# Kernel optimization log

Hardware: AMD Instinct MI355X
Metric: run time of the kernel (lower is better)

The kernel has to match this reference:

```python
import jax, jax.numpy as jnp
import numpy as np

CHEB_K = 3  # from init_kwargs


def setup_inputs() -> dict:
    key = jax.random.key(0)
    k1, k2, k3, k4 = jax.random.split(key, 4)
    B, N, C_IN, C_OUT, D = 32, 4096, 32, 64, 16
    x = jax.random.normal(k1, (B, N, C_IN), dtype=jnp.float32)
    node_embeddings = jax.random.normal(k2, (N, D), dtype=jnp.float32)
    laplacian_mx = jnp.zeros((N, N), dtype=jnp.float32)  # unused by forward
    weights_pool = jax.random.normal(k3, (D, CHEB_K, C_IN, C_OUT), dtype=jnp.float32) * 0.1
    bias_pool = jax.random.normal(k4, (D, C_OUT), dtype=jnp.float32) * 0.1
    return {
        'x': x,
        'node_embeddings': node_embeddings,
        'laplacian_mx': laplacian_mx,
        'weights_pool': weights_pool,
        'bias_pool': bias_pool,
    }


def reference(x, node_embeddings, laplacian_mx, weights_pool, bias_pool):
    N = node_embeddings.shape[0]
    # adaptive adjacency: softmax(relu(E E^T)) over rows
    supports = jax.nn.softmax(jax.nn.relu(node_embeddings @ node_embeddings.T), axis=1)
    # Chebyshev recursion T_0=I, T_1=A, T_k = 2A T_{k-1} - T_{k-2}
    support_set = [jnp.eye(N, dtype=x.dtype), supports]
    for _ in range(2, CHEB_K):
        support_set.append(2.0 * supports @ support_set[-1] - support_set[-2])
    supports_k = jnp.stack(support_set, axis=0)  # [K, N, N]
    # per-node generated weights/bias
    weights = jnp.einsum('nd,dkio->nkio', node_embeddings, weights_pool)  # [N,K,I,O]
    bias = node_embeddings @ bias_pool  # [N, O]
    # graph propagation: [K,N,N] x [B,N,I] -> [B,K,N,I] -> [B,N,K,I]
    x_g = jnp.einsum('knm,bmc->bknc', supports_k, x).transpose(0, 2, 1, 3)
    # per-node grouped GEMM
    out = jnp.einsum('bnki,nkio->bno', x_g, weights) + bias
    return out
```

## Files before the change

kernel.cpp:

```cpp
#include <hip/hip_runtime.h>
#include <hip/hip_bf16.h>

#define N_NODES 4096
#define BATCH   32
#define CIN     32
#define COUT    64
#define DEMB    16
#define NCOL    (BATCH * CIN)
#define KIO     (3 * CIN * COUT)
#define SPLITK  3

typedef __bf16 bf16x8 __attribute__((ext_vector_type(8)));
typedef float  floatx4 __attribute__((ext_vector_type(4)));

__device__ inline void load_lds16(const void* g, void* l) {
    __builtin_amdgcn_global_load_lds(
        (const __attribute__((address_space(1))) void*)g,
        (__attribute__((address_space(3))) void*)l, 16, 0, 0);
}

__global__ __launch_bounds__(256) void compute_U_kernel(
        const float* __restrict__ E, __hip_bfloat16* __restrict__ U,
        float* __restrict__ invRow) {
    const int n0   = blockIdx.x * 8;
    const int t    = threadIdx.x;
    const int lane = t & 63, wave = t >> 6;
    __shared__ float red[4][8];

    float en[8][DEMB];
#pragma unroll
    for (int r = 0; r < 8; ++r) {
        const float4* er = (const float4*)&E[(size_t)(n0 + r) * DEMB];
        const float4 a0 = er[0], a1 = er[1], a2 = er[2], a3 = er[3];
        en[r][ 0]=a0.x; en[r][ 1]=a0.y; en[r][ 2]=a0.z; en[r][ 3]=a0.w;
        en[r][ 4]=a1.x; en[r][ 5]=a1.y; en[r][ 6]=a1.z; en[r][ 7]=a1.w;
        en[r][ 8]=a2.x; en[r][ 9]=a2.y; en[r][10]=a2.z; en[r][11]=a2.w;
        en[r][12]=a3.x; en[r][13]=a3.y; en[r][14]=a3.z; en[r][15]=a3.w;
    }

    float sum[8] = {0.f, 0.f, 0.f, 0.f, 0.f, 0.f, 0.f, 0.f};

    for (int tile = 0; tile < 16; ++tile) {
        const int c = tile * 256 + t;
        const float4* em4 = (const float4*)&E[(size_t)c * DEMB];
        const float4 b0 = em4[0], b1 = em4[1], b2 = em4[2], b3 = em4[3];
        float em[DEMB];
        em[ 0]=b0.x; em[ 1]=b0.y; em[ 2]=b0.z; em[ 3]=b0.w;
        em[ 4]=b1.x; em[ 5]=b1.y; em[ 6]=b1.z; em[ 7]=b1.w;
        em[ 8]=b2.x; em[ 9]=b2.y; em[10]=b2.z; em[11]=b2.w;
        em[12]=b3.x; em[13]=b3.y; em[14]=b3.z; em[15]=b3.w;
#pragma unroll
        for (int r = 0; r < 8; ++r) {
            float dt = 0.f;
#pragma unroll
            for (int d = 0; d < DEMB; ++d) dt += en[r][d] * em[d];
            const float ev = __expf(fmaxf(dt, 0.f));
            sum[r] += ev;
            U[(size_t)(n0 + r) * N_NODES + c] = __float2bfloat16(ev);
        }
    }
#pragma unroll
    for (int r = 0; r < 8; ++r)
#pragma unroll
        for (int off = 32; off > 0; off >>= 1) sum[r] += __shfl_xor(sum[r], off);
    if (lane == 0)
#pragma unroll
        for (int r = 0; r < 8; ++r) red[wave][r] = sum[r];
    __syncthreads();
    if (t < 8)
        invRow[n0 + t] = 1.0f / (red[0][t] + red[1][t] + red[2][t] + red[3][t]);
}

__global__ __launch_bounds__(256) void transpose_kernel(
        const float* __restrict__ x,
        __hip_bfloat16* __restrict__ Xt, __hip_bfloat16* __restrict__ Bt) {
    const int m0 = blockIdx.x * 64;
    const int b  = blockIdx.y;
    const int t  = threadIdx.x;
    __shared__ float tile[64][33];
    {
        const int ml = t >> 2, cg = (t & 3) * 8;
        const float* src = &x[((size_t)b * N_NODES + (m0 + ml)) * CIN + cg];
        const float4 r0 = *(const float4*)src;
        const float4 r1 = *(const float4*)(src + 4);
        tile[ml][cg+0] = r0.x; tile[ml][cg+1] = r0.y; tile[ml][cg+2] = r0.z; tile[ml][cg+3] = r0.w;
        tile[ml][cg+4] = r1.x; tile[ml][cg+5] = r1.y; tile[ml][cg+6] = r1.z; tile[ml][cg+7] = r1.w;
    }
    __syncthreads();
    {
        const int ml = t >> 2, cg = (t & 3) * 8;
        __hip_bfloat16* dst = &Xt[(size_t)(m0 + ml) * NCOL + b * CIN + cg];
#pragma unroll
        for (int j = 0; j < 8; ++j) dst[j] = __float2bfloat16(tile[ml][cg + j]);
    }
    {
        const int c = t >> 3, mg = (t & 7) * 8;
        __hip_bfloat16* dst = &Bt[(size_t)(b * CIN + c) * N_NODES + m0 + mg];
#pragma unroll
        for (int j = 0; j < 8; ++j) dst[j] = __float2bfloat16(tile[mg + j][c]);
    }
}

__global__ __launch_bounds__(256) void gen_w_kernel(
        const float* __restrict__ E, const float* __restrict__ Wp,
        __hip_bfloat16* __restrict__ Wn) {
    const int jc = blockIdx.x * 256;
    const int nc = blockIdx.y * 64;
    const int t  = threadIdx.x;
    __shared__ float wp[DEMB][256];
    __shared__ float et[64][DEMB];
#pragma unroll
    for (int d = 0; d < DEMB; ++d) wp[d][t] = Wp[(size_t)d * KIO + jc + t];
    ((float4*)et)[t] = ((const float4*)&E[(size_t)nc * DEMB])[t];
    __syncthreads();
    float w[DEMB];
#pragma unroll
    for (int d = 0; d < DEMB; ++d) w[d] = wp[d][t];
    for (int nl = 0; nl < 64; ++nl) {
        float acc = 0.0f;
#pragma unroll
        for (int d = 0; d < DEMB; ++d) acc += et[nl][d] * w[d];
        Wn[(size_t)(nc + nl) * KIO + jc + t] = __float2bfloat16(acc);
    }
}

__global__ __launch_bounds__(256) void gemm_splitk_kernel(
        const __hip_bfloat16* __restrict__ A,
        const __hip_bfloat16* __restrict__ Bt,
        __hip_bfloat16* __restrict__ P,
        int M, int NC, int K) {
    const int t    = threadIdx.x;
    const int col0 = blockIdx.x * 128;
    const int row0 = blockIdx.y * 128;
    const int z    = blockIdx.z;
    const int iters = K >> 5;
    const int q = iters / SPLITK, rem = iters % SPLITK;
    const int it0 = z * q + (z < rem ? z : rem);
    const int it1 = it0 + q + (z < rem ? 1 : 0);

    __shared__ alignas(16) __hip_bfloat16 As[128 * 32];
    __shared__ alignas(16) __hip_bfloat16 Bs[128 * 32];
    const int lane = t & 63, wave = t >> 6;
    const int l16 = lane & 15, quad = lane >> 4;
    const int wrow = (wave >> 1) * 64, wcol = (wave & 1) * 64;

    floatx4 acc[4][4] = {};

    for (int it = it0; it < it1; ++it) {
        const int kb = it << 5;
        __syncthreads();
#pragma unroll
        for (int s = 0; s < 2; ++s) {
            const int e = s * 2048 + t * 8;
            const int r = e >> 5, ko = e & 31;
            load_lds16(&A [(size_t)(row0 + r) * K + kb + ko], &As[e]);
            load_lds16(&Bt[(size_t)(col0 + r) * K + kb + ko], &Bs[e]);
        }
        __syncthreads();
        bf16x8 af[4], bfr[4];
#pragma unroll
        for (int i = 0; i < 4; ++i)
            af[i]  = *(const bf16x8*)&As[(wrow + i * 16 + l16) * 32 + quad * 8];
#pragma unroll
        for (int i = 0; i < 4; ++i)
            bfr[i] = *(const bf16x8*)&Bs[(wcol + i * 16 + l16) * 32 + quad * 8];
#pragma unroll
        for (int i = 0; i < 4; ++i)
#pragma unroll
            for (int j = 0; j < 4; ++j)
                acc[i][j] = __builtin_amdgcn_mfma_f32_16x16x32_bf16(
                                af[i], bfr[j], acc[i][j], 0, 0, 0);
    }

    __hip_bfloat16* Pz = P + (size_t)z * M * NC;
#pragma unroll
    for (int i = 0; i < 4; ++i)
#pragma unroll
        for (int j = 0; j < 4; ++j)
#pragma unroll
            for (int r = 0; r < 4; ++r) {
                const int rg = row0 + wrow + i * 16 + quad * 4 + r;
                const int cg = col0 + wcol + j * 16 + l16;
                Pz[(size_t)rg * NC + cg] = __float2bfloat16(acc[i][j][r]);
            }
}

__global__ __launch_bounds__(256) void combine1_kernel(
        const __hip_bfloat16* __restrict__ P, const float* __restrict__ invRow,
        __hip_bfloat16* __restrict__ Y, __hip_bfloat16* __restrict__ Yt,
        int M, int NC) {
    const int c0 = blockIdx.x * 64, m0 = blockIdx.y * 64;
    const int t = threadIdx.x;
    __shared__ float tile[64][65];
    const size_t stride = (size_t)M * NC;
#pragma unroll
    for (int j = 0; j < 16; ++j) {
        const int lin = t + j * 256;
        const int r = lin >> 6, c = lin & 63;
        const size_t idx = (size_t)(m0 + r) * NC + c0 + c;
        float s = 0.f;
#pragma unroll
        for (int z = 0; z < SPLITK; ++z) s += __bfloat162float(P[idx + z * stride]);
        s *= invRow[m0 + r];
        tile[r][c] = s;
        Y[idx] = __float2bfloat16(s);
    }
    __syncthreads();
#pragma unroll
    for (int j = 0; j < 16; ++j) {
        const int lin = t + j * 256;
        const int c = lin >> 6, r = lin & 63;
        Yt[(size_t)(c0 + c) * M + m0 + r] = __float2bfloat16(tile[r][c]);
    }
}

__global__ __launch_bounds__(256) void combine2_kernel(
        const __hip_bfloat16* __restrict__ P, const float* __restrict__ invRow,
        const __hip_bfloat16* __restrict__ sub, __hip_bfloat16* __restrict__ Y2,
        int M, int NC) {
    const size_t stride = (size_t)M * NC;
    const size_t idx0 = (size_t)blockIdx.x * 4096 + threadIdx.x;
#pragma unroll
    for (int j = 0; j < 16; ++j) {
        const size_t idx = idx0 + (size_t)j * 256;
        float s = 0.f;
#pragma unroll
        for (int z = 0; z < SPLITK; ++z) s += __bfloat162float(P[idx + z * stride]);
        s *= invRow[idx >> 10];
        Y2[idx] = __float2bfloat16(2.0f * s - __bfloat162float(sub[idx]));
    }
}

__global__ __launch_bounds__(256) void final_kernel(
        const __hip_bfloat16* __restrict__ Xt, const __hip_bfloat16* __restrict__ Y1,
        const __hip_bfloat16* __restrict__ Y2, const __hip_bfloat16* __restrict__ Wn,
        const float* __restrict__ E, const float* __restrict__ bias_pool,
        float* __restrict__ out) {
    const int t    = threadIdx.x;
    const int lane = t & 63, wave = t >> 6;
    const int l16  = lane & 15, quad = lane >> 4;
    const int n    = blockIdx.x * 4 + wave;

    const __hip_bfloat16* srcs[3] = {Xt, Y1, Y2};
    const __hip_bfloat16* Wnode = Wn + (size_t)n * KIO;

    floatx4 acc[2][4] = {};

#pragma unroll
    for (int c = 0; c < 3; ++c) {
        bf16x8 af[2];
#pragma unroll
        for (int mt = 0; mt < 2; ++mt)
            af[mt] = *(const bf16x8*)&srcs[c][(size_t)n * NCOL +
                                              (mt * 16 + l16) * 32 + quad * 8];
#pragma unroll
        for (int ot = 0; ot < 4; ++ot) {
            bf16x8 bfr;
#pragma unroll
            for (int j = 0; j < 8; ++j)
                bfr[j] = (__bf16)Wnode[(size_t)(c * 32 + quad * 8 + j) * COUT +
                                       ot * 16 + l16];
#pragma unroll
            for (int mt = 0; mt < 2; ++mt)
                acc[mt][ot] = __builtin_amdgcn_mfma_f32_16x16x32_bf16(
                                  af[mt], bfr, acc[mt][ot], 0, 0, 0);
        }
    }

    float en[DEMB];
#pragma unroll
    for (int d = 0; d < DEMB; ++d) en[d] = E[(size_t)n * DEMB + d];
#pragma unroll
    for (int ot = 0; ot < 4; ++ot) {
        float bv = 0.f;
        const int o = ot * 16 + l16;
#pragma unroll
        for (int d = 0; d < DEMB; ++d) bv += en[d] * bias_pool[d * COUT + o];
#pragma unroll
        for (int mt = 0; mt < 2; ++mt)
#pragma unroll
            for (int r = 0; r < 4; ++r) {
                const int b = mt * 16 + quad * 4 + r;
                out[((size_t)b * N_NODES + n) * COUT + o] = acc[mt][ot][r] + bv;
            }
    }
}

extern "C" void kernel_launch(void* const* d_in, const int* in_sizes, int n_in,
                              void* d_out, int out_size, void* d_ws, size_t ws_size,
                              hipStream_t stream) {
    (void)in_sizes; (void)n_in; (void)out_size; (void)ws_size;
    const float* x  = (const float*)d_in[0];
    const float* E  = (const float*)d_in[1];
    const float* Wp = (const float*)d_in[3];
    const float* bp = (const float*)d_in[4];
    float* out = (float*)d_out;

    char* ws = (char*)d_ws;
    __hip_bfloat16* U   = (__hip_bfloat16*)(ws);
    __hip_bfloat16* Xt  = (__hip_bfloat16*)(ws + 33554432);
    __hip_bfloat16* Bt1 = (__hip_bfloat16*)(ws + 41943040);
    __hip_bfloat16* Y1  = (__hip_bfloat16*)(ws + 50331648);
    __hip_bfloat16* Y1t = (__hip_bfloat16*)(ws + 58720256);
    __hip_bfloat16* P   = (__hip_bfloat16*)(ws + 67108864);
    float*       invRow = (float*)(ws + 67108864 + 25165824);
    __hip_bfloat16* Wn  = (__hip_bfloat16*)(ws + 67108864);

    compute_U_kernel<<<N_NODES / 8, 256, 0, stream>>>(E, U, invRow);
    transpose_kernel<<<dim3(N_NODES / 64, BATCH), 256, 0, stream>>>(x, Xt, Bt1);
    gemm_splitk_kernel<<<dim3(NCOL / 128, N_NODES / 128, SPLITK), 256, 0, stream>>>(
        U, Bt1, P, N_NODES, NCOL, N_NODES);
    combine1_kernel<<<dim3(NCOL / 64, N_NODES / 64), 256, 0, stream>>>(
        P, invRow, Y1, Y1t, N_NODES, NCOL);
    gemm_splitk_kernel<<<dim3(NCOL / 128, N_NODES / 128, SPLITK), 256, 0, stream>>>(
        U, Y1t, P, N_NODES, NCOL, N_NODES);
    combine2_kernel<<<dim3(N_NODES * NCOL / 4096), 256, 0, stream>>>(
        P, invRow, Xt, Bt1, N_NODES, NCOL);
    gen_w_kernel<<<dim3(KIO / 256, N_NODES / 64), 256, 0, stream>>>(E, Wp, Wn);
    final_kernel<<<N_NODES / 4, 256, 0, stream>>>(Xt, Y1, Bt1, Wn, E, bp, out);
}
```

Measured before the change: 312.3 us.

## Deepen GEMM K-tile with swizzled LDS, swap grid order, pre-layout generated weights

The split-K GEMM now loads 64-wide K slices into LDS with an XOR swizzle, which avoids bank conflicts and halves the number of barriers per K step. Its grid is reordered so that consecutive blocks walk rows of U instead of columns. The per-node weight generator now writes weights already in the MFMA fragment layout as 16-byte vector stores, so the final kernel can read each B fragment with one vector load instead of eight strided scalar loads. In exchange, the GEMM uses twice the LDS per block and keeps more registers live in the weight generator.

```diff
diff --git a/kernel.cpp b/kernel.cpp
--- a/kernel.cpp
+++ b/kernel.cpp
@@ -104,23 +104,32 @@
 __global__ __launch_bounds__(256) void gen_w_kernel(
         const float* __restrict__ E, const float* __restrict__ Wp,
         __hip_bfloat16* __restrict__ Wn) {
-    const int jc = blockIdx.x * 256;
-    const int nc = blockIdx.y * 64;
+    const int c  = blockIdx.x;
+    const int n0 = blockIdx.y * 16;
     const int t  = threadIdx.x;
-    __shared__ float wp[DEMB][256];
-    __shared__ float et[64][DEMB];
-#pragma unroll
-    for (int d = 0; d < DEMB; ++d) wp[d][t] = Wp[(size_t)d * KIO + jc + t];
-    ((float4*)et)[t] = ((const float4*)&E[(size_t)nc * DEMB])[t];
-    __syncthreads();
-    float w[DEMB];
-#pragma unroll
-    for (int d = 0; d < DEMB; ++d) w[d] = wp[d][t];
-    for (int nl = 0; nl < 64; ++nl) {
-        float acc = 0.0f;
-#pragma unroll
-        for (int d = 0; d < DEMB; ++d) acc += et[nl][d] * w[d];
-        Wn[(size_t)(nc + nl) * KIO + jc + t] = __float2bfloat16(acc);
+    const int quad = t & 3, l16 = (t >> 2) & 15, ot = t >> 6;
+    const int base = (c * 32 + quad * 8) * 64 + ot * 16 + l16;
+
+    float w[DEMB][8];
+#pragma unroll
+    for (int d = 0; d < DEMB; ++d)
+#pragma unroll
+        for (int j = 0; j < 8; ++j)
+            w[d][j] = Wp[(size_t)d * KIO + base + j * 64];
+
+    for (int n = 0; n < 16; ++n) {
+        float acc[8] = {};
+#pragma unroll
+        for (int d = 0; d < DEMB; ++d) {
+            const float ed = E[(size_t)(n0 + n) * DEMB + d];
+#pragma unroll
+            for (int j = 0; j < 8; ++j) acc[j] += ed * w[d][j];
+        }
+        __hip_bfloat16 o8[8];
+#pragma unroll
+        for (int j = 0; j < 8; ++j) o8[j] = __float2bfloat16(acc[j]);
+        *(ulonglong2*)&Wn[((size_t)(n0 + n) * 3 + c) * 2048 + t * 8] =
+            *(const ulonglong2*)o8;
     }
 }
 
@@ -130,46 +139,53 @@
         __hip_bfloat16* __restrict__ P,
         int M, int NC, int K) {
     const int t    = threadIdx.x;
-    const int col0 = blockIdx.x * 128;
-    const int row0 = blockIdx.y * 128;
+    const int row0 = blockIdx.x * 128;
+    const int col0 = blockIdx.y * 128;
     const int z    = blockIdx.z;
-    const int iters = K >> 5;
+    const int iters = K >> 6;
     const int q = iters / SPLITK, rem = iters % SPLITK;
     const int it0 = z * q + (z < rem ? z : rem);
     const int it1 = it0 + q + (z < rem ? 1 : 0);
 
-    __shared__ alignas(16) __hip_bfloat16 As[128 * 32];
-    __shared__ alignas(16) __hip_bfloat16 Bs[128 * 32];
+    __shared__ alignas(16) __hip_bfloat16 As[128 * 64];
+    __shared__ alignas(16) __hip_bfloat16 Bs[128 * 64];
     const int lane = t & 63, wave = t >> 6;
     const int l16 = lane & 15, quad = lane >> 4;
     const int wrow = (wave >> 1) * 64, wcol = (wave & 1) * 64;
+    const int xr = l16 & 7;
 
     floatx4 acc[4][4] = {};
 
     for (int it = it0; it < it1; ++it) {
-        const int kb = it << 5;
+        const int kb = it << 6;
         __syncthreads();
 #pragma unroll
-        for (int s = 0; s < 2; ++s) {
-            const int e = s * 2048 + t * 8;
-            const int r = e >> 5, ko = e & 31;
-            load_lds16(&A [(size_t)(row0 + r) * K + kb + ko], &As[e]);
-            load_lds16(&Bt[(size_t)(col0 + r) * K + kb + ko], &Bs[e]);
+        for (int s = 0; s < 4; ++s) {
+            const int gi = s * 256 + t;
+            const int r  = gi >> 3;
+            const int cg = (gi & 7) ^ (r & 7);
+            load_lds16(&A [(size_t)(row0 + r) * K + kb + cg * 8], &As[gi * 8]);
+            load_lds16(&Bt[(size_t)(col0 + r) * K + kb + cg * 8], &Bs[gi * 8]);
         }
         __syncthreads();
-        bf16x8 af[4], bfr[4];
-#pragma unroll
-        for (int i = 0; i < 4; ++i)
-            af[i]  = *(const bf16x8*)&As[(wrow + i * 16 + l16) * 32 + quad * 8];
-#pragma unroll
-        for (int i = 0; i < 4; ++i)
-            bfr[i] = *(const bf16x8*)&Bs[(wcol + i * 16 + l16) * 32 + quad * 8];
-#pragma unroll
-        for (int i = 0; i < 4; ++i)
-#pragma unroll
-            for (int j = 0; j < 4; ++j)
-                acc[i][j] = __builtin_amdgcn_mfma_f32_16x16x32_bf16(
-                                af[i], bfr[j], acc[i][j], 0, 0, 0);
+#pragma unroll
+        for (int ks = 0; ks < 2; ++ks) {
+            bf16x8 af[4], bfr[4];
+#pragma unroll
+            for (int i = 0; i < 4; ++i)
+                af[i]  = *(const bf16x8*)&As[(wrow + i * 16 + l16) * 64 +
+                                             (((ks * 4 + quad) ^ xr) * 8)];
+#pragma unroll
+            for (int i = 0; i < 4; ++i)
+                bfr[i] = *(const bf16x8*)&Bs[(wcol + i * 16 + l16) * 64 +
+                                             (((ks * 4 + quad) ^ xr) * 8)];
+#pragma unroll
+            for (int i = 0; i < 4; ++i)
+#pragma unroll
+                for (int j = 0; j < 4; ++j)
+                    acc[i][j] = __builtin_amdgcn_mfma_f32_16x16x32_bf16(
+                                    af[i], bfr[j], acc[i][j], 0, 0, 0);
+        }
     }
 
     __hip_bfloat16* Pz = P + (size_t)z * M * NC;
@@ -255,11 +271,8 @@
                                               (mt * 16 + l16) * 32 + quad * 8];
 #pragma unroll
         for (int ot = 0; ot < 4; ++ot) {
-            bf16x8 bfr;
-#pragma unroll
-            for (int j = 0; j < 8; ++j)
-                bfr[j] = (__bf16)Wnode[(size_t)(c * 32 + quad * 8 + j) * COUT +
-                                       ot * 16 + l16];
+            const bf16x8 bfr = *(const bf16x8*)&Wnode[(size_t)c * 2048 +
+                                                      ot * 512 + l16 * 32 + quad * 8];
 #pragma unroll
             for (int mt = 0; mt < 2; ++mt)
                 acc[mt][ot] = __builtin_amdgcn_mfma_f32_16x16x32_bf16(
@@ -308,14 +321,14 @@
 
     compute_U_kernel<<<N_NODES / 8, 256, 0, stream>>>(E, U, invRow);
     transpose_kernel<<<dim3(N_NODES / 64, BATCH), 256, 0, stream>>>(x, Xt, Bt1);
-    gemm_splitk_kernel<<<dim3(NCOL / 128, N_NODES / 128, SPLITK), 256, 0, stream>>>(
+    gemm_splitk_kernel<<<dim3(N_NODES / 128, NCOL / 128, SPLITK), 256, 0, stream>>>(
         U, Bt1, P, N_NODES, NCOL, N_NODES);
     combine1_kernel<<<dim3(NCOL / 64, N_NODES / 64), 256, 0, stream>>>(
         P, invRow, Y1, Y1t, N_NODES, NCOL);
-    gemm_splitk_kernel<<<dim3(NCOL / 128, N_NODES / 128, SPLITK), 256, 0, stream>>>(
+    gemm_splitk_kernel<<<dim3(N_NODES / 128, NCOL / 128, SPLITK), 256, 0, stream>>>(
         U, Y1t, P, N_NODES, NCOL, N_NODES);
     combine2_kernel<<<dim3(N_NODES * NCOL / 4096), 256, 0, stream>>>(
         P, invRow, Xt, Bt1, N_NODES, NCOL);
-    gen_w_kernel<<<dim3(KIO / 256, N_NODES / 64), 256, 0, stream>>>(E, Wp, Wn);
+    gen_w_kernel<<<dim3(3, N_NODES / 16), 256, 0, stream>>>(E, Wp, Wn);
     final_kernel<<<N_NODES / 4, 256, 0, stream>>>(Xt, Y1, Bt1, Wn, E, bp, out);
 }
```

Result: no change. 310.0 us (-0.7%).
